# Kernel tuning notes

Measured on AMD Instinct MI355X. Metric: run time of the kernel, lower is better.

The kernel has to match this reference:

```python
import jax, jax.numpy as jnp
import numpy as np

NEG_BIG = -9.0e15


def masked_mean_softmax(idx):
    # softmax over a 0/-inf mask == uniform weights over positions where idx > 0
    logits = jnp.where(idx > 0, 1.0, NEG_BIG).astype(jnp.float32)
    return jax.nn.softmax(logits, axis=1)


def setup_inputs() -> dict:
    key = jax.random.key(0)
    ks = jax.random.split(key, 8)
    N_NODES, N_EDGES, EDGE_ARITY, NODE_DEG = 100000, 50000, 32, 16
    D_IN, D_OUT, TV = 128, 128, 128
    stdv = 1.0 / np.sqrt(D_IN)
    u = lambda k, shp: jax.random.uniform(k, shp, jnp.float32, -stdv, stdv)
    return {
        "x": jax.random.normal(ks[0], (N_NODES, D_IN), jnp.float32),
        "seq": jax.random.randint(ks[1], (N_EDGES, EDGE_ARITY), 0, N_NODES),
        "useq": jax.random.randint(ks[2], (N_NODES, NODE_DEG), 0, N_EDGES),
        "TextVector": jax.random.normal(ks[3], (TV,), jnp.float32),
        "weight1": u(ks[4], (D_IN, D_OUT)),
        "weight2": u(ks[5], (D_OUT, D_OUT)),
        "weight3": u(ks[6], (TV, TV)),
    }


def reference(x, seq, useq, TextVector, weight1, weight2, weight3):
    # NOTE: the torch module overwrites TextVector with weight3[0]; dropout is
    # a no-op in eval mode and is omitted here.
    tv = weight3[0]                                   # [TV]
    dot = weight3 @ tv                                # [TV]
    cos = dot / (jnp.linalg.norm(tv) * jnp.linalg.norm(weight3, axis=1))
    inter_nw = jnp.mean(cos)                          # scalar

    xw = (x @ weight1) * inter_nw                     # [N, D_OUT]

    nor = masked_mean_softmax(seq)                    # [E, A]
    adj_with_fea = xw[seq]                            # [E, A, D_OUT] gather
    edge = jnp.einsum('eac,ea->ec', adj_with_fea, nor)
    edge = jax.nn.relu(edge)
    e1 = edge @ weight2                               # [E, D_OUT]

    u_nor = masked_mean_softmax(useq)                 # [N, K]
    edge_adj = e1[useq]                               # [N, K, D_OUT] gather
    node = jnp.einsum('nkc,nk->nc', edge_adj, u_nor)  # [N, D_OUT]
    return node
```

## Files before the change

### kernel.cpp

```cpp
#include <hip/hip_runtime.h>
#include <hip/hip_fp16.h>

#define ND 100000
#define NE 50000
#define AR 32
#define DG 16
#define D  128

typedef _Float16 half8_t __attribute__((ext_vector_type(8)));
typedef _Float16 half4_t __attribute__((ext_vector_type(4)));
typedef float    f32x4_t __attribute__((ext_vector_type(4)));

#define APAD 136

__global__ __launch_bounds__(128) void k_inter(const float* __restrict__ w3,
                                               float* __restrict__ inter_out) {
    int j = threadIdx.x;
    float dot = 0.f, sq = 0.f, sq0 = 0.f;
    #pragma unroll 8
    for (int k = 0; k < D; ++k) {
        float wj = w3[j * D + k];
        float w0 = w3[k];
        dot += wj * w0;
        sq  += wj * wj;
        sq0 += w0 * w0;
    }
    float cosj = dot / (sqrtf(sq0) * sqrtf(sq));
    __shared__ float red[128];
    red[j] = cosj;
    __syncthreads();
    if (j == 0) {
        float s = 0.f;
        for (int i = 0; i < 128; ++i) s += red[i];
        inter_out[0] = s / 128.f;
    }
}

__global__ __launch_bounds__(256) void k_prep(const float* __restrict__ w1,
                                              const float* __restrict__ w2,
                                              _Float16* __restrict__ w1f,
                                              _Float16* __restrict__ w2f) {
    int o = blockIdx.x * 256 + threadIdx.x;
    int j    = o & 7;
    int lane = (o >> 3) & 63;
    int frag = o >> 9;
    int ntile = frag >> 2, ktile = frag & 3;
    int n = ntile * 16 + (lane & 15);
    int k = ktile * 32 + (lane >> 4) * 8 + j;
    w1f[o] = (_Float16)w1[k * D + n];
    w2f[o] = (_Float16)w2[k * D + n];
}

__global__ __launch_bounds__(256) void k_xw(const float* __restrict__ x,
                                            const _Float16* __restrict__ w1f_g,
                                            const float* __restrict__ inter_p,
                                            _Float16* __restrict__ xwh) {
    __shared__ _Float16 wfrag[D * D];
    __shared__ _Float16 xs[64 * APAD];
    int t = threadIdx.x;

    {
        const float4* src = (const float4*)w1f_g;
        float4* dst = (float4*)wfrag;
        #pragma unroll
        for (int i = 0; i < 8; ++i) dst[i * 256 + t] = src[i * 256 + t];
    }
    int rowbase = blockIdx.x * 64;
    #pragma unroll
    for (int p = 0; p < 8; ++p) {
        int idx = p * 1024 + t * 4;
        int r = idx >> 7, c = idx & 127;
        int grow = rowbase + r;
        float4 v = make_float4(0.f, 0.f, 0.f, 0.f);
        if (grow < ND) v = ((const float4*)x)[(size_t)grow * 32 + (c >> 2)];
        half4_t h = { (_Float16)v.x, (_Float16)v.y, (_Float16)v.z, (_Float16)v.w };
        *(half4_t*)&xs[r * APAD + c] = h;
    }
    __syncthreads();

    int wave = t >> 6, lane = t & 63;
    int quad = lane >> 4, l15 = lane & 15;
    int m0 = wave * 16;
    float inter = inter_p[0];

    half8_t a[4];
    #pragma unroll
    for (int kt = 0; kt < 4; ++kt)
        a[kt] = *(const half8_t*)&xs[(m0 + l15) * APAD + kt * 32 + quad * 8];

    #pragma unroll
    for (int nt = 0; nt < 8; ++nt) {
        f32x4_t acc = {0.f, 0.f, 0.f, 0.f};
        #pragma unroll
        for (int kt = 0; kt < 4; ++kt) {
            half8_t b = *(const half8_t*)&wfrag[((nt * 4 + kt) * 64 + lane) * 8];
            acc = __builtin_amdgcn_mfma_f32_16x16x32_f16(a[kt], b, acc, 0, 0, 0);
        }
        int col = nt * 16 + l15;
        #pragma unroll
        for (int i = 0; i < 4; ++i) {
            int grow = rowbase + m0 + quad * 4 + i;
            if (grow < ND)
                xwh[(size_t)grow * D + col] = (_Float16)(acc[i] * inter);
        }
    }
}

__global__ __launch_bounds__(256) void k_edge(const int* __restrict__ seq,
                                              const _Float16* __restrict__ xwh,
                                              const _Float16* __restrict__ w2f_g,
                                              _Float16* __restrict__ e1h) {
    __shared__ _Float16 wfrag[D * D];
    __shared__ _Float16 et[32 * APAD];
    int t = threadIdx.x;
    {
        const float4* src = (const float4*)w2f_g;
        float4* dst = (float4*)wfrag;
        #pragma unroll
        for (int i = 0; i < 8; ++i) dst[i * 256 + t] = src[i * 256 + t];
    }

    int wave = t >> 6, lane = t & 63;
    int sub = lane >> 5, il = lane & 31;
    int eb0 = blockIdx.x * 32;

    #pragma unroll
    for (int p = 0; p < 4; ++p) {
        int erow = p * 8 + wave * 2 + sub;
        int e = eb0 + erow;
        int es = (e < NE) ? e : (NE - 1);
        int sval = seq[(size_t)es * AR + il];
        unsigned long long b = __ballot(sval > 0);
        int cnt = __popcll(sub ? (unsigned long long)(b >> 32)
                               : (b & 0xffffffffULL));
        const float wuni = 1.f / 32.f;
        float wv = (cnt > 0) ? 1.f / (float)cnt : wuni;
        int c0 = il * 4;
        float a0 = 0.f, a1 = 0.f, a2 = 0.f, a3 = 0.f;
        #pragma unroll
        for (int a = 0; a < AR; ++a) {
            int srow = __shfl(sval, (sub << 5) + a, 64);
            float wa = (cnt > 0) ? ((srow > 0) ? wv : 0.f) : wuni;
            half4_t v = *(const half4_t*)(xwh + (size_t)srow * D + c0);
            a0 = fmaf(wa, (float)v[0], a0);
            a1 = fmaf(wa, (float)v[1], a1);
            a2 = fmaf(wa, (float)v[2], a2);
            a3 = fmaf(wa, (float)v[3], a3);
        }
        half4_t h = { (_Float16)fmaxf(a0, 0.f), (_Float16)fmaxf(a1, 0.f),
                      (_Float16)fmaxf(a2, 0.f), (_Float16)fmaxf(a3, 0.f) };
        *(half4_t*)&et[erow * APAD + c0] = h;
    }
    __syncthreads();

    int quad = lane >> 4, l15 = lane & 15;
    int m0 = (wave >> 1) * 16;
    int ng = (wave & 1) * 4;

    half8_t a[4];
    #pragma unroll
    for (int kt = 0; kt < 4; ++kt)
        a[kt] = *(const half8_t*)&et[(m0 + l15) * APAD + kt * 32 + quad * 8];

    #pragma unroll
    for (int nt2 = 0; nt2 < 4; ++nt2) {
        int nt = ng + nt2;
        f32x4_t acc = {0.f, 0.f, 0.f, 0.f};
        #pragma unroll
        for (int kt = 0; kt < 4; ++kt) {
            half8_t b = *(const half8_t*)&wfrag[((nt * 4 + kt) * 64 + lane) * 8];
            acc = __builtin_amdgcn_mfma_f32_16x16x32_f16(a[kt], b, acc, 0, 0, 0);
        }
        int col = nt * 16 + l15;
        #pragma unroll
        for (int i = 0; i < 4; ++i) {
            int e = eb0 + m0 + quad * 4 + i;
            if (e < NE)
                e1h[(size_t)e * D + col] = (_Float16)acc[i];
        }
    }
}

__global__ __launch_bounds__(256) void k_node(const int* __restrict__ useq,
                                              const _Float16* __restrict__ e1h,
                                              float* __restrict__ out) {
    int t = threadIdx.x;
    int wave = t >> 6, lane = t & 63;
    int n = blockIdx.x * 4 + wave;
    int hf = lane >> 5, il = lane & 31;

    int sval = useq[(size_t)n * DG + (lane & 15)];
    unsigned long long b = __ballot(sval > 0);
    int cnt = __popcll(b & 0xFFFFULL);
    const float wuni = 1.f / 16.f;
    float wv = (cnt > 0) ? 1.f / (float)cnt : wuni;

    float a0 = 0.f, a1 = 0.f, a2 = 0.f, a3 = 0.f;
    #pragma unroll
    for (int i = 0; i < 8; ++i) {
        int k = i * 2 + hf;
        int srow = __shfl(sval, k, 64);
        float wa = (cnt > 0) ? ((srow > 0) ? wv : 0.f) : wuni;
        half4_t v = *(const half4_t*)(e1h + (size_t)srow * D + il * 4);
        a0 = fmaf(wa, (float)v[0], a0);
        a1 = fmaf(wa, (float)v[1], a1);
        a2 = fmaf(wa, (float)v[2], a2);
        a3 = fmaf(wa, (float)v[3], a3);
    }
    a0 += __shfl_down(a0, 32, 64);
    a1 += __shfl_down(a1, 32, 64);
    a2 += __shfl_down(a2, 32, 64);
    a3 += __shfl_down(a3, 32, 64);
    if (lane < 32) {
        float4 o = make_float4(a0, a1, a2, a3);
        ((float4*)(out + (size_t)n * D))[il] = o;
    }
}

extern "C" void kernel_launch(void* const* d_in, const int* in_sizes, int n_in,
                              void* d_out, int out_size, void* d_ws, size_t ws_size,
                              hipStream_t stream) {
    const float* x    = (const float*)d_in[0];
    const int*   seq  = (const int*)d_in[1];
    const int*   useq = (const int*)d_in[2];
    const float* w1   = (const float*)d_in[4];
    const float* w2   = (const float*)d_in[5];
    const float* w3   = (const float*)d_in[6];
    float* out = (float*)d_out;

    _Float16* xwh   = (_Float16*)d_out;
    float*    inter = (float*)d_ws;
    _Float16* w1f   = (_Float16*)((char*)d_ws + 256);
    _Float16* w2f   = (_Float16*)((char*)d_ws + 256 + 32768);
    _Float16* e1h   = (_Float16*)((char*)d_ws + 256 + 65536);

    hipLaunchKernelGGL(k_inter, dim3(1),              dim3(128), 0, stream, w3, inter);
    hipLaunchKernelGGL(k_prep,  dim3(64),             dim3(256), 0, stream, w1, w2, w1f, w2f);
    hipLaunchKernelGGL(k_xw,    dim3((ND + 63) / 64), dim3(256), 0, stream, x, w1f, inter, xwh);
    hipLaunchKernelGGL(k_edge,  dim3((NE + 31) / 32), dim3(256), 0, stream, seq, xwh, w2f, e1h);
    hipLaunchKernelGGL(k_node,  dim3(ND / 4),         dim3(256), 0, stream, useq, e1h, out);
}
```

Baseline: 230.3 us.

## Split edge gather from GEMM and widen gather loads to 16 bytes

Merges the cosine-scalar kernel into the weight-prep kernel as an extra block, saving one launch. Splits the fused edge gather+GEMM into a dedicated gather kernel (one wave per edge, 16-byte half8 loads, cross-lane reduction) and a separate 64-row MFMA GEMM kernel reading the gathered rows from a scratch region placed after xwh in the output buffer. The node gather now handles two nodes per wave with half8 loads to raise memory-level parallelism. This costs an extra global round trip of the edge activations (NE×128 fp16) and one more launch in exchange for better gather occupancy and load width.

```diff
diff --git a/kernel.cpp b/kernel.cpp
--- a/kernel.cpp
+++ b/kernel.cpp
@@ -13,33 +13,35 @@
 
 #define APAD 136
 
-__global__ __launch_bounds__(128) void k_inter(const float* __restrict__ w3,
-                                               float* __restrict__ inter_out) {
-    int j = threadIdx.x;
-    float dot = 0.f, sq = 0.f, sq0 = 0.f;
-    #pragma unroll 8
-    for (int k = 0; k < D; ++k) {
-        float wj = w3[j * D + k];
-        float w0 = w3[k];
-        dot += wj * w0;
-        sq  += wj * wj;
-        sq0 += w0 * w0;
-    }
-    float cosj = dot / (sqrtf(sq0) * sqrtf(sq));
-    __shared__ float red[128];
-    red[j] = cosj;
-    __syncthreads();
-    if (j == 0) {
-        float s = 0.f;
-        for (int i = 0; i < 128; ++i) s += red[i];
-        inter_out[0] = s / 128.f;
-    }
-}
-
 __global__ __launch_bounds__(256) void k_prep(const float* __restrict__ w1,
                                               const float* __restrict__ w2,
+                                              const float* __restrict__ w3,
                                               _Float16* __restrict__ w1f,
-                                              _Float16* __restrict__ w2f) {
+                                              _Float16* __restrict__ w2f,
+                                              float* __restrict__ inter_out) {
+    if (blockIdx.x == 64) {
+        __shared__ float red[128];
+        int j = threadIdx.x;
+        if (j < 128) {
+            float dot = 0.f, sq = 0.f, sq0 = 0.f;
+            #pragma unroll 8
+            for (int k = 0; k < D; ++k) {
+                float wj = w3[j * D + k];
+                float w0 = w3[k];
+                dot += wj * w0;
+                sq  += wj * wj;
+                sq0 += w0 * w0;
+            }
+            red[j] = dot / (sqrtf(sq0) * sqrtf(sq));
+        }
+        __syncthreads();
+        if (j == 0) {
+            float s = 0.f;
+            for (int i = 0; i < 128; ++i) s += red[i];
+            inter_out[0] = s / 128.f;
+        }
+        return;
+    }
     int o = blockIdx.x * 256 + threadIdx.x;
     int j    = o & 7;
     int lane = (o >> 3) & 63;
@@ -106,12 +108,48 @@
     }
 }
 
-__global__ __launch_bounds__(256) void k_edge(const int* __restrict__ seq,
-                                              const _Float16* __restrict__ xwh,
-                                              const _Float16* __restrict__ w2f_g,
-                                              _Float16* __restrict__ e1h) {
+__global__ __launch_bounds__(256) void k_gather_e(const int* __restrict__ seq,
+                                                  const _Float16* __restrict__ xwh,
+                                                  _Float16* __restrict__ ea) {
+    int t = threadIdx.x;
+    int wave = t >> 6, lane = t & 63;
+    int e = blockIdx.x * 4 + wave;
+    int grp = lane >> 4, il = lane & 15;
+
+    int sval = seq[(size_t)e * AR + (lane & 31)];
+    unsigned long long b = __ballot(sval > 0);
+    int cnt = __popcll((unsigned long long)(b & 0xffffffffULL));
+    const float wuni = 1.f / 32.f;
+    float wv = (cnt > 0) ? 1.f / (float)cnt : wuni;
+
+    float acc[8] = {};
+    #pragma unroll
+    for (int i = 0; i < 8; ++i) {
+        int aslot = i * 4 + grp;
+        int srow = __shfl(sval, aslot, 64);
+        float wa = (cnt > 0) ? ((srow > 0) ? wv : 0.f) : wuni;
+        half8_t v = *(const half8_t*)(xwh + (size_t)srow * D + il * 8);
+        #pragma unroll
+        for (int jj = 0; jj < 8; ++jj) acc[jj] = fmaf(wa, (float)v[jj], acc[jj]);
+    }
+    #pragma unroll
+    for (int jj = 0; jj < 8; ++jj) {
+        acc[jj] += __shfl_down(acc[jj], 32, 64);
+        acc[jj] += __shfl_down(acc[jj], 16, 64);
+    }
+    if (lane < 16) {
+        half8_t h;
+        #pragma unroll
+        for (int jj = 0; jj < 8; ++jj) h[jj] = (_Float16)fmaxf(acc[jj], 0.f);
+        *(half8_t*)(ea + (size_t)e * D + il * 8) = h;
+    }
+}
+
+__global__ __launch_bounds__(256) void k_gemm_e(const _Float16* __restrict__ ea,
+                                                const _Float16* __restrict__ w2f_g,
+                                                _Float16* __restrict__ e1h) {
     __shared__ _Float16 wfrag[D * D];
-    __shared__ _Float16 et[32 * APAD];
+    __shared__ _Float16 et[64 * APAD];
     int t = threadIdx.x;
     {
         const float4* src = (const float4*)w2f_g;
@@ -119,43 +157,21 @@
         #pragma unroll
         for (int i = 0; i < 8; ++i) dst[i * 256 + t] = src[i * 256 + t];
     }
-
-    int wave = t >> 6, lane = t & 63;
-    int sub = lane >> 5, il = lane & 31;
-    int eb0 = blockIdx.x * 32;
-
+    int rowbase = blockIdx.x * 64;
     #pragma unroll
     for (int p = 0; p < 4; ++p) {
-        int erow = p * 8 + wave * 2 + sub;
-        int e = eb0 + erow;
-        int es = (e < NE) ? e : (NE - 1);
-        int sval = seq[(size_t)es * AR + il];
-        unsigned long long b = __ballot(sval > 0);
-        int cnt = __popcll(sub ? (unsigned long long)(b >> 32)
-                               : (b & 0xffffffffULL));
-        const float wuni = 1.f / 32.f;
-        float wv = (cnt > 0) ? 1.f / (float)cnt : wuni;
-        int c0 = il * 4;
-        float a0 = 0.f, a1 = 0.f, a2 = 0.f, a3 = 0.f;
-        #pragma unroll
-        for (int a = 0; a < AR; ++a) {
-            int srow = __shfl(sval, (sub << 5) + a, 64);
-            float wa = (cnt > 0) ? ((srow > 0) ? wv : 0.f) : wuni;
-            half4_t v = *(const half4_t*)(xwh + (size_t)srow * D + c0);
-            a0 = fmaf(wa, (float)v[0], a0);
-            a1 = fmaf(wa, (float)v[1], a1);
-            a2 = fmaf(wa, (float)v[2], a2);
-            a3 = fmaf(wa, (float)v[3], a3);
-        }
-        half4_t h = { (_Float16)fmaxf(a0, 0.f), (_Float16)fmaxf(a1, 0.f),
-                      (_Float16)fmaxf(a2, 0.f), (_Float16)fmaxf(a3, 0.f) };
-        *(half4_t*)&et[erow * APAD + c0] = h;
+        int hidx = p * 2048 + t * 8;
+        int r = hidx >> 7, c = hidx & 127;
+        int grow = rowbase + r;
+        int gs = (grow < NE) ? grow : (NE - 1);
+        half8_t v = *(const half8_t*)(ea + (size_t)gs * D + c);
+        *(half8_t*)&et[r * APAD + c] = v;
     }
     __syncthreads();
 
+    int wave = t >> 6, lane = t & 63;
     int quad = lane >> 4, l15 = lane & 15;
-    int m0 = (wave >> 1) * 16;
-    int ng = (wave & 1) * 4;
+    int m0 = wave * 16;
 
     half8_t a[4];
     #pragma unroll
@@ -163,8 +179,7 @@
         a[kt] = *(const half8_t*)&et[(m0 + l15) * APAD + kt * 32 + quad * 8];
 
     #pragma unroll
-    for (int nt2 = 0; nt2 < 4; ++nt2) {
-        int nt = ng + nt2;
+    for (int nt = 0; nt < 8; ++nt) {
         f32x4_t acc = {0.f, 0.f, 0.f, 0.f};
         #pragma unroll
         for (int kt = 0; kt < 4; ++kt) {
@@ -174,46 +189,63 @@
         int col = nt * 16 + l15;
         #pragma unroll
         for (int i = 0; i < 4; ++i) {
-            int e = eb0 + m0 + quad * 4 + i;
-            if (e < NE)
-                e1h[(size_t)e * D + col] = (_Float16)acc[i];
-        }
-    }
-}
-
-__global__ __launch_bounds__(256) void k_node(const int* __restrict__ useq,
-                                              const _Float16* __restrict__ e1h,
-                                              float* __restrict__ out) {
-    int t = threadIdx.x;
-    int wave = t >> 6, lane = t & 63;
-    int n = blockIdx.x * 4 + wave;
-    int hf = lane >> 5, il = lane & 31;
-
-    int sval = useq[(size_t)n * DG + (lane & 15)];
+            int grow = rowbase + m0 + quad * 4 + i;
+            if (grow < NE)
+                e1h[(size_t)grow * D + col] = (_Float16)acc[i];
+        }
+    }
+}
+
+__global__ __launch_bounds__(256) void k_gather_n(const int* __restrict__ useq,
+                                                  const _Float16* __restrict__ e1h,
+                                                  float* __restrict__ out) {
+    int t = threadIdx.x;
+    int wave = t >> 6, lane = t & 63;
+    int n0 = blockIdx.x * 8 + wave * 2;
+    int n1 = n0 + 1;
+    int grp = lane >> 4, il = lane & 15;
+
+    int nd = grp & 1;
+    int sval = useq[(size_t)(n0 + nd) * DG + il];
     unsigned long long b = __ballot(sval > 0);
-    int cnt = __popcll(b & 0xFFFFULL);
+    int cnt0 = __popcll((unsigned long long)(b & 0xFFFFULL));
+    int cnt1 = __popcll((unsigned long long)((b >> 16) & 0xFFFFULL));
     const float wuni = 1.f / 16.f;
-    float wv = (cnt > 0) ? 1.f / (float)cnt : wuni;
-
-    float a0 = 0.f, a1 = 0.f, a2 = 0.f, a3 = 0.f;
-    #pragma unroll
-    for (int i = 0; i < 8; ++i) {
-        int k = i * 2 + hf;
-        int srow = __shfl(sval, k, 64);
-        float wa = (cnt > 0) ? ((srow > 0) ? wv : 0.f) : wuni;
-        half4_t v = *(const half4_t*)(e1h + (size_t)srow * D + il * 4);
-        a0 = fmaf(wa, (float)v[0], a0);
-        a1 = fmaf(wa, (float)v[1], a1);
-        a2 = fmaf(wa, (float)v[2], a2);
-        a3 = fmaf(wa, (float)v[3], a3);
-    }
-    a0 += __shfl_down(a0, 32, 64);
-    a1 += __shfl_down(a1, 32, 64);
-    a2 += __shfl_down(a2, 32, 64);
-    a3 += __shfl_down(a3, 32, 64);
-    if (lane < 32) {
-        float4 o = make_float4(a0, a1, a2, a3);
-        ((float4*)(out + (size_t)n * D))[il] = o;
+    float wv0 = (cnt0 > 0) ? 1.f / (float)cnt0 : wuni;
+    float wv1 = (cnt1 > 0) ? 1.f / (float)cnt1 : wuni;
+
+    float acc0[8] = {}, acc1[8] = {};
+    #pragma unroll
+    for (int i = 0; i < 4; ++i) {
+        int slot = i * 4 + grp;
+        int s0 = __shfl(sval, slot, 64);
+        int s1 = __shfl(sval, 16 + slot, 64);
+        float w0 = (cnt0 > 0) ? ((s0 > 0) ? wv0 : 0.f) : wuni;
+        float w1 = (cnt1 > 0) ? ((s1 > 0) ? wv1 : 0.f) : wuni;
+        half8_t v0 = *(const half8_t*)(e1h + (size_t)s0 * D + il * 8);
+        half8_t v1 = *(const half8_t*)(e1h + (size_t)s1 * D + il * 8);
+        #pragma unroll
+        for (int jj = 0; jj < 8; ++jj) {
+            acc0[jj] = fmaf(w0, (float)v0[jj], acc0[jj]);
+            acc1[jj] = fmaf(w1, (float)v1[jj], acc1[jj]);
+        }
+    }
+    #pragma unroll
+    for (int jj = 0; jj < 8; ++jj) {
+        acc0[jj] += __shfl_down(acc0[jj], 32, 64);
+        acc0[jj] += __shfl_down(acc0[jj], 16, 64);
+        acc1[jj] += __shfl_down(acc1[jj], 32, 64);
+        acc1[jj] += __shfl_down(acc1[jj], 16, 64);
+    }
+    if (lane < 16) {
+        float4 o0a = make_float4(acc0[0], acc0[1], acc0[2], acc0[3]);
+        float4 o0b = make_float4(acc0[4], acc0[5], acc0[6], acc0[7]);
+        float4 o1a = make_float4(acc1[0], acc1[1], acc1[2], acc1[3]);
+        float4 o1b = make_float4(acc1[4], acc1[5], acc1[6], acc1[7]);
+        float4* p0 = (float4*)(out + (size_t)n0 * D + il * 8);
+        float4* p1 = (float4*)(out + (size_t)n1 * D + il * 8);
+        p0[0] = o0a; p0[1] = o0b;
+        p1[0] = o1a; p1[1] = o1b;
     }
 }
 
@@ -229,14 +261,15 @@
     float* out = (float*)d_out;
 
     _Float16* xwh   = (_Float16*)d_out;
+    _Float16* ea    = (_Float16*)d_out + (size_t)ND * D;
     float*    inter = (float*)d_ws;
     _Float16* w1f   = (_Float16*)((char*)d_ws + 256);
     _Float16* w2f   = (_Float16*)((char*)d_ws + 256 + 32768);
     _Float16* e1h   = (_Float16*)((char*)d_ws + 256 + 65536);
 
-    hipLaunchKernelGGL(k_inter, dim3(1),              dim3(128), 0, stream, w3, inter);
-    hipLaunchKernelGGL(k_prep,  dim3(64),             dim3(256), 0, stream, w1, w2, w1f, w2f);
-    hipLaunchKernelGGL(k_xw,    dim3((ND + 63) / 64), dim3(256), 0, stream, x, w1f, inter, xwh);
-    hipLaunchKernelGGL(k_edge,  dim3((NE + 31) / 32), dim3(256), 0, stream, seq, xwh, w2f, e1h);
-    hipLaunchKernelGGL(k_node,  dim3(ND / 4),         dim3(256), 0, stream, useq, e1h, out);
-}
+    hipLaunchKernelGGL(k_prep,     dim3(65),             dim3(256), 0, stream, w1, w2, w3, w1f, w2f, inter);
+    hipLaunchKernelGGL(k_xw,       dim3((ND + 63) / 64), dim3(256), 0, stream, x, w1f, inter, xwh);
+    hipLaunchKernelGGL(k_gather_e, dim3(NE / 4),         dim3(256), 0, stream, seq, xwh, ea);
+    hipLaunchKernelGGL(k_gemm_e,   dim3((NE + 63) / 64), dim3(256), 0, stream, ea, w2f, e1h);
+    hipLaunchKernelGGL(k_gather_n, dim3(ND / 8),         dim3(256), 0, stream, useq, e1h, out);
+}
```

Measured after the change: 232.7 us. About the same (+1.0%).
